# Performance work log

Hardware: AMD Instinct MI355X
Metric: run time of the kernel (lower is better)

The kernel has to match this reference:

```python
import jax, jax.numpy as jnp
import numpy as np


def setup_inputs() -> dict:
    key = jax.random.key(0)
    kq, kk, kv, kiq, kik = jax.random.split(key, 5)
    B, H, S, D = 2, 16, 4096, 64
    NSQ = 2048  # round(0.5 * S)
    NSK = 2048  # round(0.5 * S)
    Q = jax.random.normal(kq, (B, H, S, D), dtype=jnp.float32)
    K = jax.random.normal(kk, (B, H, S, D), dtype=jnp.float32)
    V = jax.random.normal(kv, (B, H, S, D), dtype=jnp.float32)
    mask = jnp.ones((B, S), dtype=jnp.float32)
    sample_idx_q = jnp.sort(jax.random.randint(kiq, (NSQ,), 0, S, dtype=jnp.int32))
    sample_idx_k = jax.random.randint(kik, (NSK,), 0, S, dtype=jnp.int32)
    return {"Q": Q, "K": K, "V": V, "mask": mask,
            "sample_idx_q": sample_idx_q, "sample_idx_k": sample_idx_k}


def reference(Q, K, V, mask, sample_idx_q, sample_idx_k):
    # Q,K,V: [B,H,S,D]; sample_idx_q sorted int [NSQ]; sample_idx_k int [NSK]
    S = Q.shape[-2]
    nsq = sample_idx_q.shape[0]
    nsk = sample_idx_k.shape[0]
    Qs = Q[:, :, sample_idx_q, :]            # [B,H,NSQ,D]
    Vs = V[:, :, sample_idx_k, :]            # [B,H,NSK,D]
    # NOTE: original code computes K's softmax from Q (faithful to source bug):
    Qsm = jax.nn.softmax(Qs, axis=-1)        # softmax over head_dim
    Ksm = jax.nn.softmax(Qsm, axis=-2)       # softmax over sampled seq dim
    # dot = K^T @ V : [B,H,D,D]  (requires NSQ == NSK, as in source)
    dot = jnp.einsum('bhsd,bhse->bhde', Ksm, Vs)
    ac = jnp.einsum('bhsd,bhde->bhse', Qsm, dot)  # [B,H,NSQ,D]
    scale = (S * S) / (nsq * nsk)
    ac = scale * ac + (S / nsk) * Vs
    # Serial duplicate-merge + scatter == segmented sum over duplicate q indices,
    # written into a zero tensor at the unique sampled positions.
    attn = jnp.zeros_like(V).at[:, :, sample_idx_q, :].add(ac)
    return attn
```

## Files before the change

### kernel.cpp

```cpp
#include <hip/hip_runtime.h>

constexpr int S    = 4096;
constexpr int D    = 64;
constexpr int NSQ  = 2048;
constexpr int BH   = 32;
constexpr int SD   = S * D;

constexpr int SPA  = 16;
constexpr int RPBA = NSQ / SPA;
constexpr int RPWA = RPBA / 4;
constexpr int ITA  = RPWA / 4;
constexpr int PEA  = 130;

constexpr int SPC  = 32;
constexpr int RPBC = NSQ / SPC;
constexpr int RPWC = RPBC / 4;
constexpr int ITC  = RPWC / 4;
constexpr int PQ   = 68;

using f32x16 = __attribute__((ext_vector_type(16))) float;
using s16x8  = __attribute__((ext_vector_type(8)))  short;

#define DEV static __device__ __forceinline__

DEV unsigned short f2bf(float f) {
    unsigned x = __builtin_bit_cast(unsigned, f);
    x += 0x7fffu + ((x >> 16) & 1u);
    return (unsigned short)(x >> 16);
}

DEV s16x8 load_frag(const unsigned short* p) {
    const unsigned* u = (const unsigned*)p;
    union { unsigned w[4]; s16x8 v; } r;
    r.w[0] = u[0]; r.w[1] = u[1]; r.w[2] = u[2]; r.w[3] = u[3];
    return r.v;
}

__global__ __launch_bounds__(256) void
kA(const float* __restrict__ Q, const float* __restrict__ V,
   const int* __restrict__ iq, const int* __restrict__ ik,
   float* __restrict__ Mp, float* __restrict__ Cp) {
    __shared__ unsigned short Et[64 * PEA];
    __shared__ unsigned short Vt[64 * PEA];
    __shared__ float Cl[4][256];
    __shared__ int iqL[RPBA], ikL[RPBA];

    const int bh   = blockIdx.x / SPA;
    const int sp   = blockIdx.x % SPA;
    const int lane = threadIdx.x & 63;
    const int wave = threadIdx.x >> 6;
    const int rq   = lane >> 4;
    const int c    = lane & 15;

    const int rbase = sp * RPBA;
    if (threadIdx.x < RPBA) {
        iqL[threadIdx.x] = iq[rbase + threadIdx.x];
        ikL[threadIdx.x] = ik[rbase + threadIdx.x];
    }
    __syncthreads();

    const float* Qb = Q + (size_t)bh * SD;
    const float* Vb = V + (size_t)bh * SD;

    float c4[4] = {0.f, 0.f, 0.f, 0.f};
    #pragma unroll
    for (int it = 0; it < ITA; ++it) {
        const int sl = wave * RPWA + it * 4 + rq;
        const int qi = iqL[sl];
        const int ki = ikL[sl];
        const float4 qv = *(const float4*)&Qb[qi * D + 4 * c];
        const float4 vv = *(const float4*)&Vb[ki * D + 4 * c];
        const float e0 = __expf(qv.x), e1 = __expf(qv.y),
                    e2 = __expf(qv.z), e3 = __expf(qv.w);
        float s = (e0 + e1) + (e2 + e3);
        s += __shfl_xor(s, 1); s += __shfl_xor(s, 2);
        s += __shfl_xor(s, 4); s += __shfl_xor(s, 8);
        const float inv = 1.0f / s;
        const float E0 = __expf(e0 * inv), E1 = __expf(e1 * inv),
                    E2 = __expf(e2 * inv), E3 = __expf(e3 * inv);
        c4[0] += E0; c4[1] += E1; c4[2] += E2; c4[3] += E3;
        Et[(4 * c + 0) * PEA + sl] = f2bf(E0);
        Et[(4 * c + 1) * PEA + sl] = f2bf(E1);
        Et[(4 * c + 2) * PEA + sl] = f2bf(E2);
        Et[(4 * c + 3) * PEA + sl] = f2bf(E3);
        Vt[(4 * c + 0) * PEA + sl] = f2bf(vv.x);
        Vt[(4 * c + 1) * PEA + sl] = f2bf(vv.y);
        Vt[(4 * c + 2) * PEA + sl] = f2bf(vv.z);
        Vt[(4 * c + 3) * PEA + sl] = f2bf(vv.w);
    }
    Cl[wave][lane * 4 + 0] = c4[0];
    Cl[wave][lane * 4 + 1] = c4[1];
    Cl[wave][lane * 4 + 2] = c4[2];
    Cl[wave][lane * 4 + 3] = c4[3];
    __syncthreads();

    const int d0 = (wave & 1) * 32, n0 = (wave >> 1) * 32;
    const int m  = lane & 31, h = lane >> 5;
    f32x16 acc = {0,0,0,0,0,0,0,0,0,0,0,0,0,0,0,0};
    #pragma unroll
    for (int t = 0; t < RPBA / 16; ++t) {
        s16x8 a = load_frag(&Et[(d0 + m) * PEA + t * 16 + h * 8]);
        s16x8 b = load_frag(&Vt[(n0 + m) * PEA + t * 16 + h * 8]);
        acc = __builtin_amdgcn_mfma_f32_32x32x16_bf16(a, b, acc, 0, 0, 0);
    }

    float* Mb = Mp + ((size_t)bh * SPA + sp) * 4096;
    #pragma unroll
    for (int r = 0; r < 16; ++r) {
        const int row = (r & 3) + 8 * (r >> 2) + 4 * h;
        Mb[(d0 + row) * 64 + n0 + m] = acc[r];
    }
    if (wave == 0) {
        const int cc = lane >> 2, j = lane & 3;
        float cs = 0.f;
        #pragma unroll
        for (int w = 0; w < 4; ++w)
            #pragma unroll
            for (int r = 0; r < 4; ++r)
                cs += Cl[w][(16 * r + cc) * 4 + j];
        Cp[((size_t)bh * SPA + sp) * 64 + lane] = cs;
    }
}

__global__ __launch_bounds__(256) void
kC(const float* __restrict__ Q, const float* __restrict__ V,
   const int* __restrict__ iq, const int* __restrict__ ik,
   const float* __restrict__ Mp, const float* __restrict__ Cp,
   float* __restrict__ out) {
    __shared__ unsigned short Qs[RPBC * PQ];
    __shared__ unsigned short Gt[64 * PQ];
    __shared__ float Cf[64];
    __shared__ int iqL[RPBC], ikL[RPBC];

    const int bh   = blockIdx.x / SPC;
    const int sp   = blockIdx.x % SPC;
    const int lane = threadIdx.x & 63;
    const int wave = threadIdx.x >> 6;
    const int rq   = lane >> 4;
    const int c    = lane & 15;

    const int rbase = sp * RPBC;
    if (threadIdx.x < RPBC) {
        iqL[threadIdx.x] = iq[rbase + threadIdx.x];
        ikL[threadIdx.x] = ik[rbase + threadIdx.x];
    }
    if (threadIdx.x < 64) {
        float cs = 0.f;
        #pragma unroll
        for (int p = 0; p < SPA; ++p)
            cs += Cp[((size_t)bh * SPA + p) * 64 + threadIdx.x];
        Cf[threadIdx.x] = cs;
    }
    __syncthreads();

    const float* MpB = Mp + (size_t)bh * SPA * 4096;
    #pragma unroll
    for (int k = 0; k < 4; ++k) {
        const int elb = (k * 256 + threadIdx.x) * 4;
        const int d = elb >> 6, e4 = elb & 63;
        float4 ms = {0.f, 0.f, 0.f, 0.f};
        #pragma unroll
        for (int p = 0; p < SPA; ++p) {
            const float4 t = *(const float4*)&MpB[p * 4096 + elb];
            ms.x += t.x; ms.y += t.y; ms.z += t.z; ms.w += t.w;
        }
        const float g = 4.0f / Cf[d];
        Gt[(e4 + 0) * PQ + d] = f2bf(ms.x * g);
        Gt[(e4 + 1) * PQ + d] = f2bf(ms.y * g);
        Gt[(e4 + 2) * PQ + d] = f2bf(ms.z * g);
        Gt[(e4 + 3) * PQ + d] = f2bf(ms.w * g);
    }

    const float* Qb = Q + (size_t)bh * SD;
    const float* Vb = V + (size_t)bh * SD;
    float*       Ob = out + (size_t)bh * SD;
    #pragma unroll
    for (int it = 0; it < ITC; ++it) {
        const int sl = wave * RPWC + it * 4 + rq;
        const int qi = iqL[sl];
        const float4 qv = *(const float4*)&Qb[qi * D + 4 * c];
        const float e0 = __expf(qv.x), e1 = __expf(qv.y),
                    e2 = __expf(qv.z), e3 = __expf(qv.w);
        float s = (e0 + e1) + (e2 + e3);
        s += __shfl_xor(s, 1); s += __shfl_xor(s, 2);
        s += __shfl_xor(s, 4); s += __shfl_xor(s, 8);
        const float inv = 1.0f / s;
        uint2 pk;
        pk.x = (unsigned)f2bf(e0 * inv) | ((unsigned)f2bf(e1 * inv) << 16);
        pk.y = (unsigned)f2bf(e2 * inv) | ((unsigned)f2bf(e3 * inv) << 16);
        *(uint2*)&Qs[sl * PQ + 4 * c] = pk;
    }
    __syncthreads();

    const int m0 = (wave & 1) * 32, n0 = (wave >> 1) * 32;
    const int m  = lane & 31, h = lane >> 5;
    f32x16 acc;
    #pragma unroll
    for (int r = 0; r < 16; ++r) {
        const int row = (r & 3) + 8 * (r >> 2) + 4 * h;
        const int ki  = ikL[m0 + row];
        acc[r] = 2.0f * Vb[ki * D + n0 + m];
    }
    #pragma unroll
    for (int t = 0; t < RPBC / 16; ++t) {
        s16x8 a = load_frag(&Qs[(m0 + m) * PQ + t * 16 + h * 8]);
        s16x8 b = load_frag(&Gt[(n0 + m) * PQ + t * 16 + h * 8]);
        acc = __builtin_amdgcn_mfma_f32_32x32x16_bf16(a, b, acc, 0, 0, 0);
    }
    #pragma unroll
    for (int r = 0; r < 16; ++r) {
        const int row = (r & 3) + 8 * (r >> 2) + 4 * h;
        const int qi  = iqL[m0 + row];
        atomicAdd(&Ob[qi * D + n0 + m], acc[r]);
    }
}

extern "C" void kernel_launch(void* const* d_in, const int* in_sizes, int n_in,
                              void* d_out, int out_size, void* d_ws, size_t ws_size,
                              hipStream_t stream) {
    const float* Q  = (const float*)d_in[0];
    const float* V  = (const float*)d_in[2];
    const int*   iq = (const int*)d_in[4];
    const int*   ik = (const int*)d_in[5];
    float*       out = (float*)d_out;

    float* Mp = (float*)d_ws;
    float* Cp = Mp + (size_t)BH * SPA * 4096;

    hipMemsetAsync(d_out, 0, (size_t)out_size * sizeof(float), stream);
    kA<<<BH * SPA, 256, 0, stream>>>(Q, V, iq, ik, Mp, Cp);
    kC<<<BH * SPC, 256, 0, stream>>>(Q, V, iq, ik, Mp, Cp, out);
}
```

Measured before the change: 155.8 us.

## Split reduction into separate kernel and reuse softmaxed Q from first pass

The first kernel now writes the bf16 row-softmaxed Q to workspace, so the last kernel no longer reloads Q with a gather and redoes the exp/softmax. A new middle kernel reduces the partial D×D products and column sums once per head into a bf16 G matrix, instead of every block of the last kernel repeating that 16-way reduction. The first kernel is split twice as finely (SPA 32) for more parallelism. In exchange there is one extra launch and more workspace traffic, and twice as many partials to reduce.

```diff
diff --git a/kernel.cpp b/kernel.cpp
--- a/kernel.cpp
+++ b/kernel.cpp
@@ -6,16 +6,13 @@
 constexpr int BH   = 32;
 constexpr int SD   = S * D;
 
-constexpr int SPA  = 16;
+constexpr int SPA  = 32;
 constexpr int RPBA = NSQ / SPA;
-constexpr int RPWA = RPBA / 4;
-constexpr int ITA  = RPWA / 4;
-constexpr int PEA  = 130;
+constexpr int ITA  = 4;
+constexpr int PEA  = 66;
 
 constexpr int SPC  = 32;
 constexpr int RPBC = NSQ / SPC;
-constexpr int RPWC = RPBC / 4;
-constexpr int ITC  = RPWC / 4;
 constexpr int PQ   = 68;
 
 using f32x16 = __attribute__((ext_vector_type(16))) float;
@@ -39,7 +36,8 @@
 __global__ __launch_bounds__(256) void
 kA(const float* __restrict__ Q, const float* __restrict__ V,
    const int* __restrict__ iq, const int* __restrict__ ik,
-   float* __restrict__ Mp, float* __restrict__ Cp) {
+   float* __restrict__ Mp, float* __restrict__ Cp,
+   unsigned short* __restrict__ Qsw) {
     __shared__ unsigned short Et[64 * PEA];
     __shared__ unsigned short Vt[64 * PEA];
     __shared__ float Cl[4][256];
@@ -65,7 +63,7 @@
     float c4[4] = {0.f, 0.f, 0.f, 0.f};
     #pragma unroll
     for (int it = 0; it < ITA; ++it) {
-        const int sl = wave * RPWA + it * 4 + rq;
+        const int sl = wave * 16 + it * 4 + rq;
         const int qi = iqL[sl];
         const int ki = ikL[sl];
         const float4 qv = *(const float4*)&Qb[qi * D + 4 * c];
@@ -76,8 +74,9 @@
         s += __shfl_xor(s, 1); s += __shfl_xor(s, 2);
         s += __shfl_xor(s, 4); s += __shfl_xor(s, 8);
         const float inv = 1.0f / s;
-        const float E0 = __expf(e0 * inv), E1 = __expf(e1 * inv),
-                    E2 = __expf(e2 * inv), E3 = __expf(e3 * inv);
+        const float q0 = e0 * inv, q1 = e1 * inv, q2 = e2 * inv, q3 = e3 * inv;
+        const float E0 = __expf(q0), E1 = __expf(q1),
+                    E2 = __expf(q2), E3 = __expf(q3);
         c4[0] += E0; c4[1] += E1; c4[2] += E2; c4[3] += E3;
         Et[(4 * c + 0) * PEA + sl] = f2bf(E0);
         Et[(4 * c + 1) * PEA + sl] = f2bf(E1);
@@ -87,6 +86,10 @@
         Vt[(4 * c + 1) * PEA + sl] = f2bf(vv.y);
         Vt[(4 * c + 2) * PEA + sl] = f2bf(vv.z);
         Vt[(4 * c + 3) * PEA + sl] = f2bf(vv.w);
+        uint2 pk;
+        pk.x = (unsigned)f2bf(q0) | ((unsigned)f2bf(q1) << 16);
+        pk.y = (unsigned)f2bf(q2) | ((unsigned)f2bf(q3) << 16);
+        *(uint2*)&Qsw[((size_t)bh * NSQ + rbase + sl) * 64 + 4 * c] = pk;
     }
     Cl[wave][lane * 4 + 0] = c4[0];
     Cl[wave][lane * 4 + 1] = c4[1];
@@ -103,7 +106,6 @@
         s16x8 b = load_frag(&Vt[(n0 + m) * PEA + t * 16 + h * 8]);
         acc = __builtin_amdgcn_mfma_f32_32x32x16_bf16(a, b, acc, 0, 0, 0);
     }
-
     float* Mb = Mp + ((size_t)bh * SPA + sp) * 4096;
     #pragma unroll
     for (int r = 0; r < 16; ++r) {
@@ -123,74 +125,84 @@
 }
 
 __global__ __launch_bounds__(256) void
-kC(const float* __restrict__ Q, const float* __restrict__ V,
+kB(const float* __restrict__ Mp, const float* __restrict__ Cp,
+   unsigned short* __restrict__ Gtw) {
+    __shared__ float Cf[64];
+    const int bh = blockIdx.x >> 2;
+    const int qr = blockIdx.x & 3;
+
+    if (threadIdx.x < 64) {
+        float cs = 0.f;
+        #pragma unroll 8
+        for (int p = 0; p < SPA; ++p)
+            cs += Cp[((size_t)bh * SPA + p) * 64 + threadIdx.x];
+        Cf[threadIdx.x] = cs;
+    }
+    __syncthreads();
+
+    const int l = qr * 1024 + threadIdx.x * 4;
+    const int d = l >> 6;
+    const float* MpB = Mp + (size_t)bh * SPA * 4096;
+    float4 ms = {0.f, 0.f, 0.f, 0.f};
+    #pragma unroll 8
+    for (int p = 0; p < SPA; ++p) {
+        const float4 t = *(const float4*)&MpB[p * 4096 + l];
+        ms.x += t.x; ms.y += t.y; ms.z += t.z; ms.w += t.w;
+    }
+    const float g = 4.0f / Cf[d];
+    uint2 pk;
+    pk.x = (unsigned)f2bf(ms.x * g) | ((unsigned)f2bf(ms.y * g) << 16);
+    pk.y = (unsigned)f2bf(ms.z * g) | ((unsigned)f2bf(ms.w * g) << 16);
+    *(uint2*)&Gtw[(size_t)bh * 4096 + l] = pk;
+}
+
+__global__ __launch_bounds__(256) void
+kC(const float* __restrict__ V,
    const int* __restrict__ iq, const int* __restrict__ ik,
-   const float* __restrict__ Mp, const float* __restrict__ Cp,
+   const unsigned short* __restrict__ Qsw, const unsigned short* __restrict__ Gtw,
    float* __restrict__ out) {
     __shared__ unsigned short Qs[RPBC * PQ];
     __shared__ unsigned short Gt[64 * PQ];
-    __shared__ float Cf[64];
     __shared__ int iqL[RPBC], ikL[RPBC];
 
     const int bh   = blockIdx.x / SPC;
     const int sp   = blockIdx.x % SPC;
     const int lane = threadIdx.x & 63;
     const int wave = threadIdx.x >> 6;
-    const int rq   = lane >> 4;
-    const int c    = lane & 15;
-
     const int rbase = sp * RPBC;
+
     if (threadIdx.x < RPBC) {
         iqL[threadIdx.x] = iq[rbase + threadIdx.x];
         ikL[threadIdx.x] = ik[rbase + threadIdx.x];
     }
-    if (threadIdx.x < 64) {
-        float cs = 0.f;
+
+    {
+        const int l0 = threadIdx.x * 16;
+        const int d  = l0 >> 6;
+        const uint4 w0 = *(const uint4*)&Gtw[(size_t)bh * 4096 + l0];
+        const uint4 w1 = *(const uint4*)&Gtw[(size_t)bh * 4096 + l0 + 8];
+        const unsigned wv[8] = {w0.x, w0.y, w0.z, w0.w, w1.x, w1.y, w1.z, w1.w};
+        const int e0 = l0 & 63;
         #pragma unroll
-        for (int p = 0; p < SPA; ++p)
-            cs += Cp[((size_t)bh * SPA + p) * 64 + threadIdx.x];
-        Cf[threadIdx.x] = cs;
-    }
-    __syncthreads();
-
-    const float* MpB = Mp + (size_t)bh * SPA * 4096;
-    #pragma unroll
-    for (int k = 0; k < 4; ++k) {
-        const int elb = (k * 256 + threadIdx.x) * 4;
-        const int d = elb >> 6, e4 = elb & 63;
-        float4 ms = {0.f, 0.f, 0.f, 0.f};
-        #pragma unroll
-        for (int p = 0; p < SPA; ++p) {
-            const float4 t = *(const float4*)&MpB[p * 4096 + elb];
-            ms.x += t.x; ms.y += t.y; ms.z += t.z; ms.w += t.w;
+        for (int j = 0; j < 8; ++j) {
+            Gt[(e0 + 2 * j + 0) * PQ + d] = (unsigned short)(wv[j] & 0xffffu);
+            Gt[(e0 + 2 * j + 1) * PQ + d] = (unsigned short)(wv[j] >> 16);
         }
-        const float g = 4.0f / Cf[d];
-        Gt[(e4 + 0) * PQ + d] = f2bf(ms.x * g);
-        Gt[(e4 + 1) * PQ + d] = f2bf(ms.y * g);
-        Gt[(e4 + 2) * PQ + d] = f2bf(ms.z * g);
-        Gt[(e4 + 3) * PQ + d] = f2bf(ms.w * g);
-    }
-
-    const float* Qb = Q + (size_t)bh * SD;
+    }
+    {
+        const int l0  = threadIdx.x * 16;
+        const int row = l0 >> 6, col = l0 & 63;
+        const uint4 w0 = *(const uint4*)&Qsw[((size_t)bh * NSQ + rbase) * 64 + l0];
+        const uint4 w1 = *(const uint4*)&Qsw[((size_t)bh * NSQ + rbase) * 64 + l0 + 8];
+        *(uint2*)&Qs[row * PQ + col + 0] = make_uint2(w0.x, w0.y);
+        *(uint2*)&Qs[row * PQ + col + 4] = make_uint2(w0.z, w0.w);
+        *(uint2*)&Qs[row * PQ + col + 8] = make_uint2(w1.x, w1.y);
+        *(uint2*)&Qs[row * PQ + col + 12] = make_uint2(w1.z, w1.w);
+    }
+    __syncthreads();
+
     const float* Vb = V + (size_t)bh * SD;
     float*       Ob = out + (size_t)bh * SD;
-    #pragma unroll
-    for (int it = 0; it < ITC; ++it) {
-        const int sl = wave * RPWC + it * 4 + rq;
-        const int qi = iqL[sl];
-        const float4 qv = *(const float4*)&Qb[qi * D + 4 * c];
-        const float e0 = __expf(qv.x), e1 = __expf(qv.y),
-                    e2 = __expf(qv.z), e3 = __expf(qv.w);
-        float s = (e0 + e1) + (e2 + e3);
-        s += __shfl_xor(s, 1); s += __shfl_xor(s, 2);
-        s += __shfl_xor(s, 4); s += __shfl_xor(s, 8);
-        const float inv = 1.0f / s;
-        uint2 pk;
-        pk.x = (unsigned)f2bf(e0 * inv) | ((unsigned)f2bf(e1 * inv) << 16);
-        pk.y = (unsigned)f2bf(e2 * inv) | ((unsigned)f2bf(e3 * inv) << 16);
-        *(uint2*)&Qs[sl * PQ + 4 * c] = pk;
-    }
-    __syncthreads();
 
     const int m0 = (wave & 1) * 32, n0 = (wave >> 1) * 32;
     const int m  = lane & 31, h = lane >> 5;
@@ -224,10 +236,13 @@
     const int*   ik = (const int*)d_in[5];
     float*       out = (float*)d_out;
 
-    float* Mp = (float*)d_ws;
-    float* Cp = Mp + (size_t)BH * SPA * 4096;
+    float*          Mp  = (float*)d_ws;
+    float*          Cp  = Mp + (size_t)BH * SPA * 4096;
+    unsigned short* Qsw = (unsigned short*)(Cp + (size_t)BH * SPA * 64);
+    unsigned short* Gtw = Qsw + (size_t)BH * NSQ * 64;
 
     hipMemsetAsync(d_out, 0, (size_t)out_size * sizeof(float), stream);
-    kA<<<BH * SPA, 256, 0, stream>>>(Q, V, iq, ik, Mp, Cp);
-    kC<<<BH * SPC, 256, 0, stream>>>(Q, V, iq, ik, Mp, Cp, out);
-}
+    kA<<<BH * SPA, 256, 0, stream>>>(Q, V, iq, ik, Mp, Cp, Qsw);
+    kB<<<BH * 4, 256, 0, stream>>>(Mp, Cp, Gtw);
+    kC<<<BH * SPC, 256, 0, stream>>>(V, iq, ik, Qsw, Gtw, out);
+}
```

New measurement: 156.3 us. Within noise of the previous version (+0.3%).
